# Kernel tuning notes

Hardware: AMD Instinct MI355X
Metric: run time of the kernel (lower is better)

Reference implementation:

```python
import jax, jax.numpy as jnp
import numpy as np

IN_FEATURES = 256
OUT_FEATURES = 256
GRID_SIZE = 5
SPLINE_ORDER = 3
GRID_RANGE = (-1.0, 1.0)
LN_EPS = 1e-5


def _make_grid():
    h = (GRID_RANGE[1] - GRID_RANGE[0]) / GRID_SIZE
    n_knots = GRID_SIZE + 2 * SPLINE_ORDER + 1  # 12
    return jnp.linspace(GRID_RANGE[0] - h * SPLINE_ORDER,
                        GRID_RANGE[1] + h * SPLINE_ORDER,
                        n_knots, dtype=jnp.float32)


def setup_inputs() -> dict:
    key = jax.random.key(0)
    k1, k2, k3 = jax.random.split(key, 3)
    N = 65536
    # kaiming_uniform_(nonlinearity='linear'): bound = sqrt(3/fan_in)
    b1 = np.sqrt(3.0 / IN_FEATURES)
    fan_sp = IN_FEATURES * (GRID_SIZE + SPLINE_ORDER)
    b2 = np.sqrt(3.0 / fan_sp)
    return {
        "x": jax.random.normal(k1, (N, IN_FEATURES), dtype=jnp.float32),
        "grid": _make_grid(),
        "base_weight": jax.random.uniform(k2, (OUT_FEATURES, IN_FEATURES), jnp.float32, -b1, b1),
        "spline_weight": jax.random.uniform(k3, (OUT_FEATURES, IN_FEATURES, GRID_SIZE + SPLINE_ORDER), jnp.float32, -b2, b2),
        "ln_gamma": jnp.ones((OUT_FEATURES,), jnp.float32),
        "ln_beta": jnp.zeros((OUT_FEATURES,), jnp.float32),
        "prelu_a": jnp.full((1,), 0.25, jnp.float32),
    }


def reference(x, grid, base_weight, spline_weight, ln_gamma, ln_beta, prelu_a):
    # base branch: exact GELU then linear (matches nn.GELU() + F.linear)
    base_out = jnp.einsum('ni,oi->no', jax.nn.gelu(x, approximate=False), base_weight)

    # Cox-de Boor B-spline basis recursion. grid is identical per feature in
    # the original ([in, 12] expand of a 1D linspace) so we broadcast the 1D grid.
    xu = x[:, :, None]                                   # [N, in, 1]
    bases = ((xu >= grid[:-1]) & (xu < grid[1:])).astype(x.dtype)  # [N, in, 11]
    for k in range(1, SPLINE_ORDER + 1):
        left = grid[:-(k + 1)]
        right = grid[k:-1]
        delta = jnp.where(right == left, jnp.ones_like(right), right - left)
        bases = ((xu - left) / delta * bases[:, :, :-1]
                 + (grid[k + 1:] - xu) / (grid[k + 1:] - grid[1:-k]) * bases[:, :, 1:])
    # bases: [N, in, grid_size + spline_order]

    spline_out = jnp.einsum('nig,oig->no', bases, spline_weight)

    y = base_out + spline_out
    mu = jnp.mean(y, axis=-1, keepdims=True)
    var = jnp.mean(jnp.square(y - mu), axis=-1, keepdims=True)
    y = (y - mu) * jax.lax.rsqrt(var + LN_EPS) * ln_gamma + ln_beta
    # PReLU with a single shared slope (nn.PReLU default)
    return jnp.where(y >= 0, y, prelu_a[0] * y)
```

## Files before the change

kernel.cpp:

```cpp
#include <hip/hip_runtime.h>
#include <hip/hip_bf16.h>
#include <math.h>
#include <stdint.h>

typedef __attribute__((ext_vector_type(8))) short short8;
typedef __attribute__((ext_vector_type(4))) float f32x4;

#define BM 128
#define NKT 36
#define A_BYTES (BM * 128)
#define LDS_TOTAL (2 * A_BYTES)

__device__ __forceinline__ unsigned short f2bf(float f) {
    union { float f; unsigned u; } c; c.f = f;
    unsigned u = c.u;
    unsigned r = u + 0x7fffu + ((u >> 16) & 1u);
    return (unsigned short)(r >> 16);
}

__device__ __forceinline__ float gelu_exact(float x) {
    return 0.5f * x * (1.0f + erff(x * 0.7071067811865475f));
}

__device__ __forceinline__ int swz(int row, int u) {
    return row * 128 + ((u ^ (row & 7)) << 4);
}

__global__ void kan_prep_w(const float* __restrict__ bw, const float* __restrict__ sw,
                           unsigned short* __restrict__ Wf) {
    int U = blockIdx.x * 256 + threadIdx.x;
    if (U >= NKT * 2048) return;
    int kt = U >> 11, rem = U & 2047;
    int wcq = rem >> 9, rem2 = rem & 511;
    int i = rem2 >> 6;
    int lane = rem2 & 63;
    int o = wcq * 64 + (i & 3) * 16 + (lane & 15);
    int k0 = kt * 64 + ((i >> 2) * 4 + (lane >> 4)) * 8;
    unsigned short pk[8];
#pragma unroll
    for (int e = 0; e < 8; ++e) {
        int kk = k0 + e;
        float v = (kk < 256) ? bw[o * 256 + kk] : sw[o * 2048 + (kk - 256)];
        pk[e] = f2bf(v);
    }
    *(short8*)(Wf + (size_t)U * 8) = *(short8*)pk;
}

__device__ __forceinline__ short8 spline_row(float xv) {
    float xi = (xv + 2.2f) * 2.5f;
    float fi = floorf(xi);
    float tt = xi - fi;
    float s1 = 1.0f - tt;
    float t2 = tt * tt, t3 = t2 * tt;
    float w0 = s1 * s1 * s1 * (1.0f / 6.0f);
    float w1 = 0.5f * t3 - t2 + (2.0f / 3.0f);
    float w2 = -0.5f * t3 + 0.5f * t2 + 0.5f * tt + (1.0f / 6.0f);
    float w3 = t3 * (1.0f / 6.0f);
    uint64_t Wp = (uint64_t)f2bf(w0) | ((uint64_t)f2bf(w1) << 16)
                | ((uint64_t)f2bf(w2) << 32) | ((uint64_t)f2bf(w3) << 48);
    int b = 16 * ((int)fi - 3);
    uint64_t L = (b >= 0 && b < 64) ? (Wp << b)
               : ((b < 0 && b > -64) ? (Wp >> (-b)) : 0ull);
    uint64_t H = (b >= 64 && b < 128) ? (Wp << (b - 64))
               : ((b > 0 && b < 64) ? (Wp >> (64 - b)) : 0ull);
    union { uint64_t q[2]; short8 v; } rr;
    rr.q[0] = L; rr.q[1] = H;
    return rr.v;
}

__global__ __launch_bounds__(512)
void kan_fused(
    const float* __restrict__ X, const unsigned short* __restrict__ Wf,
    const float* __restrict__ gamma, const float* __restrict__ beta,
    const float* __restrict__ prelu_a, float* __restrict__ OUT)
{
    extern __shared__ __align__(16) unsigned char lds[];

    const int t = threadIdx.x;
    const int row0 = blockIdx.x * BM;
    const int wid = t >> 6, lane = t & 63;
    const int wr = wid >> 2, wc = wid & 3;
    const int lcol = lane & 15, q = lane >> 4;
    const int srow = t >> 3, scol = t & 7;

    f32x4 acc[4][4];
#pragma unroll
    for (int m = 0; m < 4; ++m)
#pragma unroll
        for (int n = 0; n < 4; ++n) acc[m][n] = (f32x4){0.f, 0.f, 0.f, 0.f};

    const unsigned short* wlane = Wf + ((size_t)wc * 512 + lane) * 8;

#pragma unroll
    for (int rep = 0; rep < 2; ++rep) {
        const float* xp = X + (size_t)(row0 + srow + rep * 64) * 256 + scol * 8;
        float4 v0 = *(const float4*)xp;
        float4 v1 = *(const float4*)(xp + 4);
        float vv[8] = {v0.x, v0.y, v0.z, v0.w, v1.x, v1.y, v1.z, v1.w};
        unsigned short pk[8];
#pragma unroll
        for (int j = 0; j < 8; ++j) pk[j] = f2bf(gelu_exact(vv[j]));
        *(short8*)(lds + swz(srow + rep * 64, scol)) = *(short8*)pk;
    }
    __syncthreads();

    for (int kt = 0; kt < NKT; ++kt) {
        unsigned char* A_cur = lds + (kt & 1) * A_BYTES;
        unsigned char* A_nxt = lds + ((kt + 1) & 1) * A_BYTES;
        const bool has_next = (kt + 1 < NKT);
        const bool nxt_gelu = (kt + 1 < 4);

        float xs[2];
        if (has_next && !nxt_gelu) {
            const int ibase = (kt + 1 - 4) * 8;
#pragma unroll
            for (int rep = 0; rep < 2; ++rep)
                xs[rep] = X[(size_t)(row0 + srow + rep * 64) * 256 + ibase + scol];
        }

#pragma unroll
        for (int kh = 0; kh < 2; ++kh) {
            const unsigned short* wsrc = wlane + ((size_t)kt * 2048 + kh * 256) * 8;
            short8 wv4[4];
#pragma unroll
            for (int n = 0; n < 4; ++n)
                wv4[n] = *(const short8*)(wsrc + n * 512);
            short8 af[4];
#pragma unroll
            for (int m = 0; m < 4; ++m)
                af[m] = *(const short8*)(A_cur + swz(wr * 64 + m * 16 + lcol, kh * 4 + q));
#pragma unroll
            for (int m = 0; m < 4; ++m)
#pragma unroll
                for (int n = 0; n < 4; ++n)
                    acc[m][n] = __builtin_amdgcn_mfma_f32_16x16x32_bf16(
                        af[m], wv4[n], acc[m][n], 0, 0, 0);
        }

        if (has_next) {
            if (nxt_gelu) {
#pragma unroll
                for (int rep = 0; rep < 2; ++rep) {
                    const float* xp = X + (size_t)(row0 + srow + rep * 64) * 256
                                    + (kt + 1) * 64 + scol * 8;
                    float4 v0 = *(const float4*)xp;
                    float4 v1 = *(const float4*)(xp + 4);
                    float vv[8] = {v0.x, v0.y, v0.z, v0.w, v1.x, v1.y, v1.z, v1.w};
                    unsigned short pk[8];
#pragma unroll
                    for (int j = 0; j < 8; ++j) pk[j] = f2bf(gelu_exact(vv[j]));
                    *(short8*)(A_nxt + swz(srow + rep * 64, scol)) = *(short8*)pk;
                }
            } else {
#pragma unroll
                for (int rep = 0; rep < 2; ++rep)
                    *(short8*)(A_nxt + swz(srow + rep * 64, scol)) = spline_row(xs[rep]);
            }
        }
        __syncthreads();
    }

    float* stats = (float*)lds;
#pragma unroll
    for (int m = 0; m < 4; ++m) {
#pragma unroll
        for (int r = 0; r < 4; ++r) {
            float s = 0.f, s2 = 0.f;
#pragma unroll
            for (int n = 0; n < 4; ++n) { float v = acc[m][n][r]; s += v; s2 += v * v; }
#pragma unroll
            for (int msk = 1; msk < 16; msk <<= 1) {
                s  += __shfl_xor(s,  msk, 64);
                s2 += __shfl_xor(s2, msk, 64);
            }
            if ((lane & 15) == (m * 4 + r)) {
                int row = wr * 64 + m * 16 + q * 4 + r;
                stats[row * 8 + wc]     = s;
                stats[row * 8 + 4 + wc] = s2;
            }
        }
    }
    __syncthreads();

    const float apr = prelu_a[0];
    float gv[4], bv[4];
#pragma unroll
    for (int n = 0; n < 4; ++n) {
        int col = wc * 64 + n * 16 + lcol;
        gv[n] = gamma[col]; bv[n] = beta[col];
    }
#pragma unroll
    for (int m = 0; m < 4; ++m) {
#pragma unroll
        for (int r = 0; r < 4; ++r) {
            int row = wr * 64 + m * 16 + q * 4 + r;
            f32x4 sv = *(const f32x4*)(stats + row * 8);
            f32x4 qv = *(const f32x4*)(stats + row * 8 + 4);
            float mu  = (sv[0] + sv[1] + sv[2] + sv[3]) * (1.0f / 256.0f);
            float ex2 = (qv[0] + qv[1] + qv[2] + qv[3]) * (1.0f / 256.0f);
            float rs = rsqrtf(ex2 - mu * mu + 1e-5f);
            float* op = OUT + (size_t)(row0 + row) * 256;
#pragma unroll
            for (int n = 0; n < 4; ++n) {
                int col = wc * 64 + n * 16 + lcol;
                float y = (acc[m][n][r] - mu) * rs * gv[n] + bv[n];
                op[col] = (y >= 0.f) ? y : apr * y;
            }
        }
    }
}

extern "C" void kernel_launch(void* const* d_in, const int* in_sizes, int n_in,
                              void* d_out, int out_size, void* d_ws, size_t ws_size,
                              hipStream_t stream) {
    const float* x  = (const float*)d_in[0];
    const float* bw = (const float*)d_in[2];
    const float* sw = (const float*)d_in[3];
    const float* g  = (const float*)d_in[4];
    const float* be = (const float*)d_in[5];
    const float* pa = (const float*)d_in[6];
    float* out = (float*)d_out;
    unsigned short* Wf = (unsigned short*)d_ws;

    hipFuncSetAttribute((const void*)kan_fused,
                        hipFuncAttributeMaxDynamicSharedMemorySize, LDS_TOTAL);

    const int Nrows = in_sizes[0] / 256;
    kan_fused;
    kan_prep_w<<<(NKT * 2048 + 255) / 256, 256, 0, stream>>>(bw, sw, Wf);
    kan_fused<<<Nrows / BM, 512, LDS_TOTAL, stream>>>(x, Wf, g, be, pa, out);
}
```

Before: 149.4 us.

## Double row tile to 256 and prefetch next weight tile into registers

Raises the row tile from 128 to 256 rows, using 1024-thread blocks with 16 waves, and remaps the staging threads so each covers one row and two column chunks. All eight weight fragments for the next K tile are loaded into registers during the current tile's MFMA work, instead of being loaded just before each MFMA group. __syncthreads is replaced by an inline s_waitcnt lgkmcnt(0) plus s_barrier. The aim is to hide global weight-load latency and halve weight traffic per output row. The cost is higher register pressure, and only 256 workgroups are launched, which can leave CUs with poor load balance.

```diff
diff --git a/kernel.cpp b/kernel.cpp
--- a/kernel.cpp
+++ b/kernel.cpp
@@ -6,7 +6,7 @@
 typedef __attribute__((ext_vector_type(8))) short short8;
 typedef __attribute__((ext_vector_type(4))) float f32x4;
 
-#define BM 128
+#define BM 256
 #define NKT 36
 #define A_BYTES (BM * 128)
 #define LDS_TOTAL (2 * A_BYTES)
@@ -68,7 +68,7 @@
     return rr.v;
 }
 
-__global__ __launch_bounds__(512)
+__global__ __launch_bounds__(1024)
 void kan_fused(
     const float* __restrict__ X, const unsigned short* __restrict__ Wf,
     const float* __restrict__ gamma, const float* __restrict__ beta,
@@ -81,7 +81,7 @@
     const int wid = t >> 6, lane = t & 63;
     const int wr = wid >> 2, wc = wid & 3;
     const int lcol = lane & 15, q = lane >> 4;
-    const int srow = t >> 3, scol = t & 7;
+    const int srow = t >> 2, sil = (t & 3) << 1;
 
     f32x4 acc[4][4];
 #pragma unroll
@@ -91,18 +91,22 @@
 
     const unsigned short* wlane = Wf + ((size_t)wc * 512 + lane) * 8;
 
+    short8 wv[8];
+#pragma unroll
+    for (int i = 0; i < 8; ++i)
+        wv[i] = *(const short8*)(wlane + i * 512);
 #pragma unroll
     for (int rep = 0; rep < 2; ++rep) {
-        const float* xp = X + (size_t)(row0 + srow + rep * 64) * 256 + scol * 8;
+        const float* xp = X + (size_t)(row0 + srow) * 256 + (sil + rep) * 8;
         float4 v0 = *(const float4*)xp;
         float4 v1 = *(const float4*)(xp + 4);
         float vv[8] = {v0.x, v0.y, v0.z, v0.w, v1.x, v1.y, v1.z, v1.w};
         unsigned short pk[8];
 #pragma unroll
         for (int j = 0; j < 8; ++j) pk[j] = f2bf(gelu_exact(vv[j]));
-        *(short8*)(lds + swz(srow + rep * 64, scol)) = *(short8*)pk;
-    }
-    __syncthreads();
+        *(short8*)(lds + swz(srow, sil + rep)) = *(short8*)pk;
+    }
+    asm volatile("s_waitcnt lgkmcnt(0)\n\ts_barrier" ::: "memory");
 
     for (int kt = 0; kt < NKT; ++kt) {
         unsigned char* A_cur = lds + (kt & 1) * A_BYTES;
@@ -115,16 +119,11 @@
             const int ibase = (kt + 1 - 4) * 8;
 #pragma unroll
             for (int rep = 0; rep < 2; ++rep)
-                xs[rep] = X[(size_t)(row0 + srow + rep * 64) * 256 + ibase + scol];
+                xs[rep] = X[(size_t)(row0 + srow) * 256 + ibase + sil + rep];
         }
 
 #pragma unroll
         for (int kh = 0; kh < 2; ++kh) {
-            const unsigned short* wsrc = wlane + ((size_t)kt * 2048 + kh * 256) * 8;
-            short8 wv4[4];
-#pragma unroll
-            for (int n = 0; n < 4; ++n)
-                wv4[n] = *(const short8*)(wsrc + n * 512);
             short8 af[4];
 #pragma unroll
             for (int m = 0; m < 4; ++m)
@@ -134,30 +133,35 @@
 #pragma unroll
                 for (int n = 0; n < 4; ++n)
                     acc[m][n] = __builtin_amdgcn_mfma_f32_16x16x32_bf16(
-                        af[m], wv4[n], acc[m][n], 0, 0, 0);
+                        af[m], wv[kh * 4 + n], acc[m][n], 0, 0, 0);
         }
 
         if (has_next) {
+            const unsigned short* wsrc = wlane + (size_t)(kt + 1) * 2048 * 8;
+#pragma unroll
+            for (int i = 0; i < 8; ++i)
+                wv[i] = *(const short8*)(wsrc + i * 512);
+
             if (nxt_gelu) {
 #pragma unroll
                 for (int rep = 0; rep < 2; ++rep) {
-                    const float* xp = X + (size_t)(row0 + srow + rep * 64) * 256
-                                    + (kt + 1) * 64 + scol * 8;
+                    const float* xp = X + (size_t)(row0 + srow) * 256
+                                    + (kt + 1) * 64 + (sil + rep) * 8;
                     float4 v0 = *(const float4*)xp;
                     float4 v1 = *(const float4*)(xp + 4);
                     float vv[8] = {v0.x, v0.y, v0.z, v0.w, v1.x, v1.y, v1.z, v1.w};
                     unsigned short pk[8];
 #pragma unroll
                     for (int j = 0; j < 8; ++j) pk[j] = f2bf(gelu_exact(vv[j]));
-                    *(short8*)(A_nxt + swz(srow + rep * 64, scol)) = *(short8*)pk;
+                    *(short8*)(A_nxt + swz(srow, sil + rep)) = *(short8*)pk;
                 }
             } else {
 #pragma unroll
                 for (int rep = 0; rep < 2; ++rep)
-                    *(short8*)(A_nxt + swz(srow + rep * 64, scol)) = spline_row(xs[rep]);
-            }
-        }
-        __syncthreads();
+                    *(short8*)(A_nxt + swz(srow, sil + rep)) = spline_row(xs[rep]);
+            }
+        }
+        asm volatile("s_waitcnt lgkmcnt(0)\n\ts_barrier" ::: "memory");
     }
 
     float* stats = (float*)lds;
@@ -226,7 +230,6 @@
                         hipFuncAttributeMaxDynamicSharedMemorySize, LDS_TOTAL);
 
     const int Nrows = in_sizes[0] / 256;
-    kan_fused;
     kan_prep_w<<<(NKT * 2048 + 255) / 256, 256, 0, stream>>>(bw, sw, Wf);
-    kan_fused<<<Nrows / BM, 512, LDS_TOTAL, stream>>>(x, Wf, g, be, pa, out);
-}
+    kan_fused<<<Nrows / BM, 1024, LDS_TOTAL, stream>>>(x, Wf, g, be, pa, out);
+}
```

Result: slower. 202.1 us (+35.2%).
